# Kernel optimization log

Hardware: AMD Instinct MI355X
Metric: run time of the kernel (lower is better)

The kernel has to match this reference:

```python
import jax, jax.numpy as jnp
import numpy as np

N = 100_000   # nodes
E = 1_600_000 # edges
V = 100_000   # vocab
G = 256       # graphs in batch
D = 64        # emb/hidden dim


def setup_inputs() -> dict:
    key = jax.random.key(0)
    ks = jax.random.split(key, 12)
    x_tokens = jax.random.randint(ks[0], (N, 1), 0, V)
    edge_index = jax.random.randint(ks[1], (2, E), 0, N)
    batch = jnp.sort(jax.random.randint(ks[2], (N,), 0, G))
    s = 0.02
    return {
        "x_tokens": x_tokens,
        "edge_index": edge_index,
        "batch": batch,
        "emb_table": jax.random.normal(ks[3], (V, D), jnp.float32) * s,
        "W0": jax.random.normal(ks[4], (D, D), jnp.float32) * s,
        "b0": jnp.zeros((D,), jnp.float32),
        "W1": jax.random.normal(ks[5], (D, D), jnp.float32) * s,
        "b1": jnp.zeros((D,), jnp.float32),
        "W2": jax.random.normal(ks[6], (D, D), jnp.float32) * s,
        "b2": jnp.zeros((D,), jnp.float32),
        "Wc1": jax.random.normal(ks[7], (2 * D, D), jnp.float32) * s,
        "bc1": jnp.zeros((D,), jnp.float32),
        "Wc2": jax.random.normal(ks[8], (D, 2), jnp.float32) * s,
        "bc2": jnp.zeros((2,), jnp.float32),
    }


def _gcn_norm(edge_index, n_nodes):
    # add self loops, compute symmetric normalization coefficients
    loop = jnp.arange(n_nodes, dtype=edge_index.dtype)
    src = jnp.concatenate([edge_index[0], loop])
    dst = jnp.concatenate([edge_index[1], loop])
    deg = jax.ops.segment_sum(jnp.ones_like(dst, jnp.float32), dst, num_segments=n_nodes)
    dinv = jnp.where(deg > 0, deg ** -0.5, 0.0)
    norm = dinv[src] * dinv[dst]  # [E+N]
    return src, dst, norm


def _gcn_conv(x, W, b, src, dst, norm, n_nodes):
    x = x @ W                                   # [N, D]
    msg = x[src] * norm[:, None]                # gather + scale, [E+N, D]
    out = jax.ops.segment_sum(msg, dst, num_segments=n_nodes)
    return out + b


def reference(x_tokens, edge_index, batch, emb_table, W0, b0, W1, b1, W2, b2, Wc1, bc1, Wc2, bc2):
    n = x_tokens.shape[0]
    src, dst, norm = _gcn_norm(edge_index, n)
    x = emb_table[x_tokens[:, 0]]               # [N, D]
    for W, b in ((W0, b0), (W1, b1), (W2, b2)):
        x = jax.nn.relu(_gcn_conv(x, W, b, src, dst, norm, n))
    # dual pooling over graph ids
    cnt = jax.ops.segment_sum(jnp.ones((n,), x.dtype), batch, num_segments=G)
    h_sum = jax.ops.segment_sum(x, batch, num_segments=G)
    h_mean = h_sum / jnp.maximum(cnt, 1.0)[:, None]
    h_max = jax.ops.segment_max(x, batch, num_segments=G)
    h_max = jnp.where(jnp.isfinite(h_max), h_max, 0.0)
    h = jnp.concatenate([h_mean, h_max], axis=-1)   # [G, 2D]
    logits = jax.nn.relu(h @ Wc1 + bc1) @ Wc2 + bc2  # [G, 2]
    return logits
```

## Files before the change

kernel.cpp:

```cpp
#include <hip/hip_runtime.h>
#include <hip/hip_fp16.h>
#include <math.h>


#define BKT_LOG 9
#define BKT (1 << BKT_LOG)
#define CHUNK 4096

typedef _Float16 h2 __attribute__((ext_vector_type(2)));
typedef _Float16 f16x4 __attribute__((ext_vector_type(4)));
typedef _Float16 f16x8 __attribute__((ext_vector_type(8)));
typedef float f32x2 __attribute__((ext_vector_type(2)));
typedef float f32x4 __attribute__((ext_vector_type(4)));

union HU { unsigned u; h2 h; };
__device__ inline h2 h2bits(unsigned u) { HU x; x.u = u; return x.h; }

#if __has_builtin(__builtin_amdgcn_fdot2)
#define FDOT2(a, b, c) __builtin_amdgcn_fdot2((a), (b), (c), false)
#else
__device__ inline float FDOT2(h2 a, h2 b, float c) {
  return (float)a.x * (float)b.x + (float)a.y * (float)b.y + c;
}
#endif

#define MASK_X 0x00003C00u
#define MASK_Y 0x3C000000u

__device__ inline void acc4c(uint2 v, float& a0, float& a1, float& a2, float& a3) {
  h2 lo = h2bits(v.x), hi = h2bits(v.y);
  a0 = FDOT2(lo, h2bits(MASK_X), a0);
  a1 = FDOT2(lo, h2bits(MASK_Y), a1);
  a2 = FDOT2(hi, h2bits(MASK_X), a2);
  a3 = FDOT2(hi, h2bits(MASK_Y), a3);
}

#if __has_builtin(__builtin_amdgcn_cvt_pk_f32_fp8) && __has_builtin(__builtin_amdgcn_cvt_pk_fp8_f32)
#define HW_FP8 1
#else
#define HW_FP8 0
#endif

__device__ inline float fp8dec_sw(unsigned b) {
  unsigned s = (b >> 7) & 1, e = (b >> 3) & 15, m = b & 7;
  float v;
  if (e == 0) v = (float)m * 0.001953125f;
  else v = __uint_as_float(((e + 120u) << 23) | (m << 20));
  return s ? -v : v;
}
__device__ inline unsigned fp8enc_sw(float f) {
  unsigned s = (__float_as_uint(f) >> 31) << 7;
  float a = fabsf(f);
  if (!(a < 448.f)) return s | 0x7E;
  if (a < 0.0009765625f) return s;
  int e; float m = frexpf(a, &e);
  int E = e + 6;
  unsigned q;
  if (E <= 0) {
    q = (unsigned)lrintf(a * 512.f);
    if (q >= 8) return s | 0x08;
    return s | q;
  }
  q = (unsigned)lrintf((m * 2.f - 1.f) * 8.f);
  if (q == 8) { q = 0; E++; if (E > 15) return s | 0x7E; }
  return s | ((unsigned)E << 3) | q;
}

__device__ inline void acc4fp8(unsigned v, float& a0, float& a1, float& a2, float& a3) {
#if HW_FP8
  f32x2 lo = __builtin_amdgcn_cvt_pk_f32_fp8((int)v, false);
  f32x2 hi = __builtin_amdgcn_cvt_pk_f32_fp8((int)v, true);
  a0 += lo[0]; a1 += lo[1]; a2 += hi[0]; a3 += hi[1];
#else
  a0 += fp8dec_sw(v & 255u);
  a1 += fp8dec_sw((v >> 8) & 255u);
  a2 += fp8dec_sw((v >> 16) & 255u);
  a3 += fp8dec_sw((v >> 24) & 255u);
#endif
}

__device__ inline unsigned pk4fp8(float f0, float f1, float f2, float f3) {
#if HW_FP8
  int t = __builtin_amdgcn_cvt_pk_fp8_f32(f0, f1, 0, false);
  return (unsigned)__builtin_amdgcn_cvt_pk_fp8_f32(f2, f3, t, true);
#else
  return fp8enc_sw(f0) | (fp8enc_sw(f1) << 8) | (fp8enc_sw(f2) << 16) | (fp8enc_sw(f3) << 24);
#endif
}

template <bool F8>
__device__ inline void rows8(const unsigned char* __restrict__ xh, int my,
                             int e0, int e1, int f, int4 iA, int4 iB,
                             float& a0, float& a1, float& a2, float& a3) {
  if (F8) {
    unsigned v0 = 0, v1 = 0, v2 = 0, v3 = 0, v4 = 0, v5 = 0, v6 = 0, v7 = 0;
    if (my + 0 >= e0 && my + 0 < e1) v0 = *(const unsigned*)(xh + ((size_t)(unsigned)iA.x << 6) + f * 4);
    if (my + 1 >= e0 && my + 1 < e1) v1 = *(const unsigned*)(xh + ((size_t)(unsigned)iA.y << 6) + f * 4);
    if (my + 2 >= e0 && my + 2 < e1) v2 = *(const unsigned*)(xh + ((size_t)(unsigned)iA.z << 6) + f * 4);
    if (my + 3 >= e0 && my + 3 < e1) v3 = *(const unsigned*)(xh + ((size_t)(unsigned)iA.w << 6) + f * 4);
    if (my + 4 >= e0 && my + 4 < e1) v4 = *(const unsigned*)(xh + ((size_t)(unsigned)iB.x << 6) + f * 4);
    if (my + 5 >= e0 && my + 5 < e1) v5 = *(const unsigned*)(xh + ((size_t)(unsigned)iB.y << 6) + f * 4);
    if (my + 6 >= e0 && my + 6 < e1) v6 = *(const unsigned*)(xh + ((size_t)(unsigned)iB.z << 6) + f * 4);
    if (my + 7 >= e0 && my + 7 < e1) v7 = *(const unsigned*)(xh + ((size_t)(unsigned)iB.w << 6) + f * 4);
    acc4fp8(v0, a0, a1, a2, a3);
    acc4fp8(v1, a0, a1, a2, a3);
    acc4fp8(v2, a0, a1, a2, a3);
    acc4fp8(v3, a0, a1, a2, a3);
    acc4fp8(v4, a0, a1, a2, a3);
    acc4fp8(v5, a0, a1, a2, a3);
    acc4fp8(v6, a0, a1, a2, a3);
    acc4fp8(v7, a0, a1, a2, a3);
  } else {
    uint2 v0 = {0,0}, v1 = {0,0}, v2 = {0,0}, v3 = {0,0};
    uint2 v4 = {0,0}, v5 = {0,0}, v6 = {0,0}, v7 = {0,0};
    if (my + 0 >= e0 && my + 0 < e1) v0 = *(const uint2*)(xh + ((size_t)(unsigned)iA.x << 7) + f * 8);
    if (my + 1 >= e0 && my + 1 < e1) v1 = *(const uint2*)(xh + ((size_t)(unsigned)iA.y << 7) + f * 8);
    if (my + 2 >= e0 && my + 2 < e1) v2 = *(const uint2*)(xh + ((size_t)(unsigned)iA.z << 7) + f * 8);
    if (my + 3 >= e0 && my + 3 < e1) v3 = *(const uint2*)(xh + ((size_t)(unsigned)iA.w << 7) + f * 8);
    if (my + 4 >= e0 && my + 4 < e1) v4 = *(const uint2*)(xh + ((size_t)(unsigned)iB.x << 7) + f * 8);
    if (my + 5 >= e0 && my + 5 < e1) v5 = *(const uint2*)(xh + ((size_t)(unsigned)iB.y << 7) + f * 8);
    if (my + 6 >= e0 && my + 6 < e1) v6 = *(const uint2*)(xh + ((size_t)(unsigned)iB.z << 7) + f * 8);
    if (my + 7 >= e0 && my + 7 < e1) v7 = *(const uint2*)(xh + ((size_t)(unsigned)iB.w << 7) + f * 8);
    acc4c(v0, a0, a1, a2, a3);
    acc4c(v1, a0, a1, a2, a3);
    acc4c(v2, a0, a1, a2, a3);
    acc4c(v3, a0, a1, a2, a3);
    acc4c(v4, a0, a1, a2, a3);
    acc4c(v5, a0, a1, a2, a3);
    acc4c(v6, a0, a1, a2, a3);
    acc4c(v7, a0, a1, a2, a3);
  }
}

__global__ __launch_bounds__(256) void k_wcvt(const float* __restrict__ W0,
                                              const float* __restrict__ W1,
                                              const float* __restrict__ W2,
                                              _Float16* __restrict__ Wf,
                                              int* __restrict__ gcur,
                                              float* __restrict__ hz, int hzn) {
  if (blockIdx.x < 3) {
    const float* W = (blockIdx.x == 0) ? W0 : (blockIdx.x == 1) ? W1 : W2;
    _Float16* out = Wf + blockIdx.x * 4096;
    for (int i = threadIdx.x; i < 4096; i += 256) {
      int c = i >> 10, s = (i >> 9) & 1, l = (i >> 3) & 63, j = i & 7;
      int k = 32 * s + 8 * (l >> 4) + j;
      int ncol = 16 * c + (l & 15);
      out[i] = (_Float16)W[k * 64 + ncol];
    }
  } else if (blockIdx.x == 3) {
    gcur[threadIdx.x] = 0;
  } else {
    for (int i = threadIdx.x; i < hzn; i += 256) hz[i] = 0.f;
  }
}

__global__ __launch_bounds__(256) void k_part(const int* __restrict__ src,
                                              const int* __restrict__ dst,
                                              int* __restrict__ gcur,
                                              int* __restrict__ ebuf,
                                              int E, int S) {
  __shared__ int pk[CHUNK];
  __shared__ unsigned short bk[CHUNK];
  __shared__ unsigned short sp[CHUNK];
  __shared__ int h[256], sc[256], base[256], cur[256];
  int tid = threadIdx.x;
  long c0 = (long)blockIdx.x * CHUNK;
  int m = (int)min((long)CHUNK, (long)E - c0);
  h[tid] = 0;
  __syncthreads();
  for (int i = tid; i < m; i += 256) {
    int s = src[c0 + i];
    int d = dst[c0 + i];
    int b = d >> BKT_LOG;
    pk[i] = ((d & (BKT - 1)) << 17) | s;
    bk[i] = (unsigned short)b;
    atomicAdd(&h[b], 1);
  }
  __syncthreads();
  int hv = h[tid];
  if (hv) base[tid] = atomicAdd(&gcur[tid], hv);
  sc[tid] = hv;
  __syncthreads();
  for (int d = 1; d < 256; d <<= 1) {
    int t = (tid >= d) ? sc[tid - d] : 0;
    __syncthreads();
    sc[tid] += t;
    __syncthreads();
  }
  cur[tid] = sc[tid] - hv;
  __syncthreads();
  for (int i = tid; i < m; i += 256) {
    int p = atomicAdd(&cur[bk[i]], 1);
    sp[p] = (unsigned short)i;
  }
  __syncthreads();
  for (int j = tid; j < m; j += 256) {
    int lo = 0, hi = 255;
    while (lo < hi) { int mid = (lo + hi) >> 1; if (sc[mid] > j) hi = mid; else lo = mid + 1; }
    int b = lo;
    int rel = j - (sc[b] - h[b]);
    int gpos = base[b] + rel;
    if (gpos < S)
      ebuf[(size_t)b * S + gpos] = pk[sp[j]];
  }
}

__global__ __launch_bounds__(512) void k_bplace(const int* __restrict__ ebuf,
                                                const int* __restrict__ gcur,
                                                int* __restrict__ off,
                                                int* __restrict__ eend,
                                                int* __restrict__ csrc,
                                                float* __restrict__ dinv,
                                                int N, int S) {
  __shared__ int s[512];
  __shared__ int cur[512];
  int b = blockIdx.x, tid = threadIdx.x;
  int n0 = b << BKT_LOG;
  int nn = min(BKT, N - n0);
  int e0 = b * S;
  int cnt = min(gcur[b], S - nn);
  s[tid] = (tid < nn) ? 1 : 0;
  __syncthreads();
  for (int e = tid; e < cnt; e += 512) atomicAdd(&s[ebuf[e0 + e] >> 17], 1);
  __syncthreads();
  int degws = s[tid];
  for (int d = 1; d < 512; d <<= 1) {
    int t = (tid >= d) ? s[tid - d] : 0;
    __syncthreads();
    s[tid] += t;
    __syncthreads();
  }
  int excl = s[tid] - degws;
  if (tid < nn) {
    off[n0 + tid] = e0 + excl;
    eend[n0 + tid] = e0 + excl + degws;
    dinv[n0 + tid] = 1.0f / sqrtf((float)degws);
    csrc[e0 + excl] = n0 + tid;
  }
  cur[tid] = excl + ((tid < nn) ? 1 : 0);
  __syncthreads();
  for (int e = tid; e < cnt; e += 512) {
    int p = ebuf[e0 + e];
    int pos = e0 + atomicAdd(&cur[p >> 17], 1);
    csrc[pos] = p & 0x1FFFF;
  }
}

template <bool EMB, bool F8>
__global__ __launch_bounds__(256) void k_mfmamm(const _Float16* __restrict__ y,
                                                const int* __restrict__ tok,
                                                const float* __restrict__ emb,
                                                const _Float16* __restrict__ Wf,
                                                const float* __restrict__ dinv,
                                                float scale,
                                                unsigned char* __restrict__ xh,
                                                int n) {
  __shared__ _Float16 lds[4 * 16 * 72];
  int w = threadIdx.x >> 6, l = threadIdx.x & 63;
  int m = l & 15, q = l >> 4;
  int rbase = blockIdx.x * 64 + w * 16;

  f16x8 a0, a1;
  if (EMB) {
    int node = min(rbase + m, n - 1);
    const float* er = emb + (size_t)tok[node] * 64;
    float4 v0 = *(const float4*)(er + q * 8);
    float4 v1 = *(const float4*)(er + q * 8 + 4);
    float4 v2 = *(const float4*)(er + 32 + q * 8);
    float4 v3 = *(const float4*)(er + 32 + q * 8 + 4);
    a0[0] = (_Float16)v0.x; a0[1] = (_Float16)v0.y; a0[2] = (_Float16)v0.z; a0[3] = (_Float16)v0.w;
    a0[4] = (_Float16)v1.x; a0[5] = (_Float16)v1.y; a0[6] = (_Float16)v1.z; a0[7] = (_Float16)v1.w;
    a1[0] = (_Float16)v2.x; a1[1] = (_Float16)v2.y; a1[2] = (_Float16)v2.z; a1[3] = (_Float16)v2.w;
    a1[4] = (_Float16)v3.x; a1[5] = (_Float16)v3.y; a1[6] = (_Float16)v3.z; a1[7] = (_Float16)v3.w;
  } else {
    int node = rbase + m;
    const _Float16* yr = y + ((size_t)(unsigned)node << 6);
    a0 = *(const f16x8*)(yr + q * 8);
    a1 = *(const f16x8*)(yr + 32 + q * 8);
  }
  float4 d4 = *(const float4*)(dinv + rbase + q * 4);

  const f16x8* wf = (const f16x8*)Wf + l;
  f32x4 acc[4];
#pragma unroll
  for (int c = 0; c < 4; c++) {
    f32x4 z = {0.f, 0.f, 0.f, 0.f};
    z = __builtin_amdgcn_mfma_f32_16x16x32_f16(a0, wf[(c * 2 + 0) * 64], z, 0, 0, 0);
    z = __builtin_amdgcn_mfma_f32_16x16x32_f16(a1, wf[(c * 2 + 1) * 64], z, 0, 0, 0);
    acc[c] = z;
  }

  const float ds[4] = {d4.x * scale, d4.y * scale, d4.z * scale, d4.w * scale};
  _Float16* ldw = lds + w * 16 * 72;
#pragma unroll
  for (int c = 0; c < 4; c++)
#pragma unroll
    for (int r = 0; r < 4; r++)
      ldw[(q * 4 + r) * 72 + c * 16 + m] = (_Float16)(acc[c][r] * ds[r]);
  __syncthreads();

  int row2 = l & 15, c2 = l >> 4;
  int node = rbase + row2;
  if (node < n) {
    if (F8) {
      const _Float16* sp16 = ldw + row2 * 72 + c2 * 16;
      unsigned wds[4];
#pragma unroll
      for (int k = 0; k < 4; k++)
        wds[k] = pk4fp8((float)sp16[4 * k + 0], (float)sp16[4 * k + 1],
                        (float)sp16[4 * k + 2], (float)sp16[4 * k + 3]);
      uint4 ov; ov.x = wds[0]; ov.y = wds[1]; ov.z = wds[2]; ov.w = wds[3];
      *(uint4*)(xh + ((size_t)(unsigned)node << 6) + c2 * 16) = ov;
    } else {
      const uint4* s4 = (const uint4*)(ldw + row2 * 72 + c2 * 16);
      uint4 v0 = s4[0], v1 = s4[1];
      uint4* dst = (uint4*)(xh + ((size_t)(unsigned)node << 7) + c2 * 32);
      dst[0] = v0;
      dst[1] = v1;
    }
  }
}

template <bool F8>
__global__ __launch_bounds__(256) void k_aggregate(const int* __restrict__ off,
                                                   const int* __restrict__ eend,
                                                   const int* __restrict__ csrc,
                                                   const float* __restrict__ dinv,
                                                   const unsigned char* __restrict__ xh,
                                                   const float* __restrict__ bias,
                                                   float invs,
                                                   _Float16* __restrict__ outp,
                                                   int n, int stride) {
  int lane = threadIdx.x & 63;
  int p = lane >> 4;
  int f = lane & 15;
  int t = __builtin_amdgcn_readfirstlane(blockIdx.x * 4 + (threadIdx.x >> 6));
  if (t >= n) return;

  int e0 = off[t], e1 = eend[t];
  int4 iA = {0, 0, 0, 0}, iB = {0, 0, 0, 0};
  {
    int my = (e0 & ~7) + p * 8;
    if (my < e1) iA = *(const int4*)(csrc + my);
    if (my + 4 < e1) iB = *(const int4*)(csrc + my + 4);
  }
  int tn = t + stride;
  int e0n = 0, e1n = 0;
  if (tn < n) { e0n = off[tn]; e1n = eend[tn]; }

  while (true) {
    int4 iAn = {0, 0, 0, 0}, iBn = {0, 0, 0, 0};
    if (tn < n) {
      int myn = (e0n & ~7) + p * 8;
      if (myn < e1n) iAn = *(const int4*)(csrc + myn);
      if (myn + 4 < e1n) iBn = *(const int4*)(csrc + myn + 4);
    }
    int tnn = tn + stride;
    int e0nn = 0, e1nn = 0;
    if (tnn < n) { e0nn = off[tnn]; e1nn = eend[tnn]; }

    float a0 = 0.f, a1 = 0.f, a2 = 0.f, a3 = 0.f;
    int base0 = e0 & ~7;
    rows8<F8>(xh, base0 + p * 8, e0, e1, f, iA, iB, a0, a1, a2, a3);
    for (int base = base0 + 32; base < e1; base += 32) {
      int my = base + p * 8;
      int4 jA = {0, 0, 0, 0}, jB = {0, 0, 0, 0};
      if (my < e1) jA = *(const int4*)(csrc + my);
      if (my + 4 < e1) jB = *(const int4*)(csrc + my + 4);
      rows8<F8>(xh, my, e0, e1, f, jA, jB, a0, a1, a2, a3);
    }

    a0 += __shfl_xor(a0, 16); a0 += __shfl_xor(a0, 32);
    a1 += __shfl_xor(a1, 16); a1 += __shfl_xor(a1, 32);
    a2 += __shfl_xor(a2, 16); a2 += __shfl_xor(a2, 32);
    a3 += __shfl_xor(a3, 16); a3 += __shfl_xor(a3, 32);
    if (p == 0) {
      float sc = dinv[t] * invs;
      float4 bb = *(const float4*)(bias + f * 4);
      f16x4 hv;
      hv[0] = (_Float16)(fmaxf(a0 * sc + bb.x, 0.f) * 4096.f);
      hv[1] = (_Float16)(fmaxf(a1 * sc + bb.y, 0.f) * 4096.f);
      hv[2] = (_Float16)(fmaxf(a2 * sc + bb.z, 0.f) * 4096.f);
      hv[3] = (_Float16)(fmaxf(a3 * sc + bb.w, 0.f) * 4096.f);
      *(f16x4*)((char*)outp + ((size_t)(unsigned)t << 7) + f * 8) = hv;
    }

    if (tn >= n) break;
    t = tn; e0 = e0n; e1 = e1n; iA = iAn; iB = iBn;
    tn = tnn; e0n = e0nn; e1n = e1nn;
  }
}

__global__ __launch_bounds__(256) void k_pool(const _Float16* __restrict__ x,
                                              const int* __restrict__ batch,
                                              float* __restrict__ hsum,
                                              float* __restrict__ hmax,
                                              int* __restrict__ cntg,
                                              int n) {
  int wid = (blockIdx.x * blockDim.x + threadIdx.x) >> 6;
  int lane = threadIdx.x & 63;
  int i0 = wid * 64;
  if (i0 >= n) return;
  int i1 = min(i0 + 64, n);
  int batch_l = (i0 + lane < n) ? batch[i0 + lane] : 0;
  float gsum = 0.f, gmax = 0.f;
  int cur = __shfl(batch_l, 0);
  int c = 0;
  for (int i = i0; i < i1; i++) {
    int g = __shfl(batch_l, i - i0);
    if (g != cur) {
      atomicAdd(&hsum[cur * 64 + lane], gsum);
      atomicMax((int*)&hmax[cur * 64 + lane], __float_as_int(gmax));
      if (lane == 0) atomicAdd(&cntg[cur], c);
      gsum = 0.f; gmax = 0.f; c = 0; cur = g;
    }
    float v = (float)x[((size_t)(unsigned)i << 6) + lane];
    gsum += v;
    gmax = fmaxf(gmax, v);
    c++;
  }
  atomicAdd(&hsum[cur * 64 + lane], gsum);
  atomicMax((int*)&hmax[cur * 64 + lane], __float_as_int(gmax));
  if (lane == 0) atomicAdd(&cntg[cur], c);
}

__global__ __launch_bounds__(64) void k_cls(const float* __restrict__ hsum,
                                            const float* __restrict__ hmax,
                                            const int* __restrict__ cnt,
                                            const float* __restrict__ Wc1,
                                            const float* __restrict__ bc1,
                                            const float* __restrict__ Wc2,
                                            const float* __restrict__ bc2,
                                            float* __restrict__ out) {
  __shared__ float h[128];
  __shared__ float hid[64];
  int g = blockIdx.x, j = threadIdx.x;
  int c = cnt[g];
  float cf = (float)(c > 0 ? c : 1);
  h[j] = hsum[g * 64 + j] / cf * (1.0f / 4096.0f);
  h[64 + j] = hmax[g * 64 + j] * (1.0f / 4096.0f);
  __syncthreads();
  float acc = bc1[j];
  for (int k = 0; k < 128; k++) acc += h[k] * Wc1[k * 64 + j];
  hid[j] = fmaxf(acc, 0.f);
  __syncthreads();
  if (j < 2) {
    float a = bc2[j];
    for (int k = 0; k < 64; k++) a += hid[k] * Wc2[k * 2 + j];
    out[g * 2 + j] = a;
  }
}

extern "C" void kernel_launch(void* const* d_in, const int* in_sizes, int n_in,
                              void* d_out, int out_size, void* d_ws, size_t ws_size,
                              hipStream_t stream) {
  const int N = in_sizes[0];
  const int E = in_sizes[1] / 2;
  const int G = out_size / 2;
  const int B = (N + BKT - 1) >> BKT_LOG;
  const int Npad = (N + 63) & ~63;
  const int S = ((((E + B - 1) / B) * 3 / 2 + 256) + 7) & ~7;

  const int* tok   = (const int*)d_in[0];
  const int* ei    = (const int*)d_in[1];
  const int* batch = (const int*)d_in[2];
  const float* emb = (const float*)d_in[3];
  const float* W0 = (const float*)d_in[4];  const float* b0 = (const float*)d_in[5];
  const float* W1 = (const float*)d_in[6];  const float* b1 = (const float*)d_in[7];
  const float* W2 = (const float*)d_in[8];  const float* b2 = (const float*)d_in[9];
  const float* Wc1 = (const float*)d_in[10]; const float* bc1 = (const float*)d_in[11];
  const float* Wc2 = (const float*)d_in[12]; const float* bc2 = (const float*)d_in[13];
  const int* srcp = ei;
  const int* dstp = ei + E;

  int* off    = (int*)d_ws;
  int* eend   = off + N;
  float* dinv = (float*)(eend + N);
  int* gcur   = (int*)(dinv + Npad);
  _Float16* Wf = (_Float16*)(gcur + 256);
  int* csrc   = (int*)(Wf + 3 * 4096);
  unsigned char* xh = (unsigned char*)(csrc + (size_t)B * S);
  _Float16* y  = (_Float16*)(xh + (size_t)Npad * 128);
  int* ebuf   = (int*)y;
  float* hsum = (float*)(y + (size_t)Npad * 64);
  float* hmax = hsum + (size_t)G * 64;
  int*   cntg = (int*)(hmax + (size_t)G * 64);

  auto cdiv = [](long a, long b) { return (int)((a + b - 1) / b); };
  const int aggBlocks = 2048;
  const int aggStride = aggBlocks * 4;

  k_wcvt<<<5, 256, 0, stream>>>(W0, W1, W2, Wf, gcur, hsum, G * 129);

  k_part<<<cdiv(E, CHUNK), 256, 0, stream>>>(srcp, dstp, gcur, ebuf, E, S);
  k_bplace<<<B, 512, 0, stream>>>(ebuf, gcur, off, eend, csrc, dinv, N, S);

  k_mfmamm<true, true><<<cdiv(N, 64), 256, 0, stream>>>(nullptr, tok, emb, Wf, dinv, 256.f, xh, N);
  k_aggregate<true><<<aggBlocks, 256, 0, stream>>>(off, eend, csrc, dinv, xh, b0, 1.f / 256.f, y, N, aggStride);

  k_mfmamm<false, true><<<cdiv(N, 64), 256, 0, stream>>>(y, nullptr, nullptr, Wf + 4096, dinv, 1.0f, xh, N);
  k_aggregate<true><<<aggBlocks, 256, 0, stream>>>(off, eend, csrc, dinv, xh, b1, 1.f / 4096.f, y, N, aggStride);

  k_mfmamm<false, false><<<cdiv(N, 64), 256, 0, stream>>>(y, nullptr, nullptr, Wf + 8192, dinv, 1.f / 16.f, xh, N);
  k_aggregate<false><<<aggBlocks, 256, 0, stream>>>(off, eend, csrc, dinv, xh, b2, 1.f / 256.f, y, N, aggStride);

  k_pool<<<cdiv(N, 256), 256, 0, stream>>>(y, batch, hsum, hmax, cntg, N);

  k_cls<<<G, 64, 0, stream>>>(hsum, hmax, cntg, Wc1, bc1, Wc2, bc2, (float*)d_out);
}
```

Before: 304.6 us.

## Fuse graph pooling into final aggregate via atomics and count nodes in bplace

Removes the separate pooling kernel by having the last aggregation layer atomically accumulate per-graph sum and max directly from each node's activations, skipping the fp16 write and reread of the final node features. Node counts per graph are computed with atomics in the CSR placement kernel instead. This trades a launch and a pass over node features for many contended per-node global atomics on a small set of graph addresses, since sorted batch ids make neighboring nodes target the same locations.

```diff
diff --git a/kernel.cpp b/kernel.cpp
--- a/kernel.cpp
+++ b/kernel.cpp
@@ -207,10 +207,12 @@
 
 __global__ __launch_bounds__(512) void k_bplace(const int* __restrict__ ebuf,
                                                 const int* __restrict__ gcur,
+                                                const int* __restrict__ batch,
                                                 int* __restrict__ off,
                                                 int* __restrict__ eend,
                                                 int* __restrict__ csrc,
                                                 float* __restrict__ dinv,
+                                                int* __restrict__ cntg,
                                                 int N, int S) {
   __shared__ int s[512];
   __shared__ int cur[512];
@@ -236,6 +238,7 @@
     eend[n0 + tid] = e0 + excl + degws;
     dinv[n0 + tid] = 1.0f / sqrtf((float)degws);
     csrc[e0 + excl] = n0 + tid;
+    atomicAdd(&cntg[batch[n0 + tid]], 1);
   }
   cur[tid] = excl + ((tid < nn) ? 1 : 0);
   __syncthreads();
@@ -321,7 +324,7 @@
   }
 }
 
-template <bool F8>
+template <bool F8, bool POOL>
 __global__ __launch_bounds__(256) void k_aggregate(const int* __restrict__ off,
                                                    const int* __restrict__ eend,
                                                    const int* __restrict__ csrc,
@@ -330,6 +333,9 @@
                                                    const float* __restrict__ bias,
                                                    float invs,
                                                    _Float16* __restrict__ outp,
+                                                   const int* __restrict__ batch,
+                                                   float* __restrict__ hsum,
+                                                   float* __restrict__ hmax,
                                                    int n, int stride) {
   int lane = threadIdx.x & 63;
   int p = lane >> 4;
@@ -377,51 +383,36 @@
     if (p == 0) {
       float sc = dinv[t] * invs;
       float4 bb = *(const float4*)(bias + f * 4);
-      f16x4 hv;
-      hv[0] = (_Float16)(fmaxf(a0 * sc + bb.x, 0.f) * 4096.f);
-      hv[1] = (_Float16)(fmaxf(a1 * sc + bb.y, 0.f) * 4096.f);
-      hv[2] = (_Float16)(fmaxf(a2 * sc + bb.z, 0.f) * 4096.f);
-      hv[3] = (_Float16)(fmaxf(a3 * sc + bb.w, 0.f) * 4096.f);
-      *(f16x4*)((char*)outp + ((size_t)(unsigned)t << 7) + f * 8) = hv;
+      float v0 = fmaxf(a0 * sc + bb.x, 0.f) * 4096.f;
+      float v1 = fmaxf(a1 * sc + bb.y, 0.f) * 4096.f;
+      float v2 = fmaxf(a2 * sc + bb.z, 0.f) * 4096.f;
+      float v3 = fmaxf(a3 * sc + bb.w, 0.f) * 4096.f;
+      if (POOL) {
+        int g = batch[t];
+        float* hs = hsum + g * 64 + f * 4;
+        int* hm = (int*)(hmax + g * 64 + f * 4);
+        atomicAdd(hs + 0, v0);
+        atomicAdd(hs + 1, v1);
+        atomicAdd(hs + 2, v2);
+        atomicAdd(hs + 3, v3);
+        atomicMax(hm + 0, __float_as_int(v0));
+        atomicMax(hm + 1, __float_as_int(v1));
+        atomicMax(hm + 2, __float_as_int(v2));
+        atomicMax(hm + 3, __float_as_int(v3));
+      } else {
+        f16x4 hv;
+        hv[0] = (_Float16)v0;
+        hv[1] = (_Float16)v1;
+        hv[2] = (_Float16)v2;
+        hv[3] = (_Float16)v3;
+        *(f16x4*)((char*)outp + ((size_t)(unsigned)t << 7) + f * 8) = hv;
+      }
     }
 
     if (tn >= n) break;
     t = tn; e0 = e0n; e1 = e1n; iA = iAn; iB = iBn;
     tn = tnn; e0n = e0nn; e1n = e1nn;
   }
-}
-
-__global__ __launch_bounds__(256) void k_pool(const _Float16* __restrict__ x,
-                                              const int* __restrict__ batch,
-                                              float* __restrict__ hsum,
-                                              float* __restrict__ hmax,
-                                              int* __restrict__ cntg,
-                                              int n) {
-  int wid = (blockIdx.x * blockDim.x + threadIdx.x) >> 6;
-  int lane = threadIdx.x & 63;
-  int i0 = wid * 64;
-  if (i0 >= n) return;
-  int i1 = min(i0 + 64, n);
-  int batch_l = (i0 + lane < n) ? batch[i0 + lane] : 0;
-  float gsum = 0.f, gmax = 0.f;
-  int cur = __shfl(batch_l, 0);
-  int c = 0;
-  for (int i = i0; i < i1; i++) {
-    int g = __shfl(batch_l, i - i0);
-    if (g != cur) {
-      atomicAdd(&hsum[cur * 64 + lane], gsum);
-      atomicMax((int*)&hmax[cur * 64 + lane], __float_as_int(gmax));
-      if (lane == 0) atomicAdd(&cntg[cur], c);
-      gsum = 0.f; gmax = 0.f; c = 0; cur = g;
-    }
-    float v = (float)x[((size_t)(unsigned)i << 6) + lane];
-    gsum += v;
-    gmax = fmaxf(gmax, v);
-    c++;
-  }
-  atomicAdd(&hsum[cur * 64 + lane], gsum);
-  atomicMax((int*)&hmax[cur * 64 + lane], __float_as_int(gmax));
-  if (lane == 0) atomicAdd(&cntg[cur], c);
 }
 
 __global__ __launch_bounds__(64) void k_cls(const float* __restrict__ hsum,
@@ -493,18 +484,16 @@
   k_wcvt<<<5, 256, 0, stream>>>(W0, W1, W2, Wf, gcur, hsum, G * 129);
 
   k_part<<<cdiv(E, CHUNK), 256, 0, stream>>>(srcp, dstp, gcur, ebuf, E, S);
-  k_bplace<<<B, 512, 0, stream>>>(ebuf, gcur, off, eend, csrc, dinv, N, S);
+  k_bplace<<<B, 512, 0, stream>>>(ebuf, gcur, batch, off, eend, csrc, dinv, cntg, N, S);
 
   k_mfmamm<true, true><<<cdiv(N, 64), 256, 0, stream>>>(nullptr, tok, emb, Wf, dinv, 256.f, xh, N);
-  k_aggregate<true><<<aggBlocks, 256, 0, stream>>>(off, eend, csrc, dinv, xh, b0, 1.f / 256.f, y, N, aggStride);
+  k_aggregate<true, false><<<aggBlocks, 256, 0, stream>>>(off, eend, csrc, dinv, xh, b0, 1.f / 256.f, y, nullptr, nullptr, nullptr, N, aggStride);
 
   k_mfmamm<false, true><<<cdiv(N, 64), 256, 0, stream>>>(y, nullptr, nullptr, Wf + 4096, dinv, 1.0f, xh, N);
-  k_aggregate<true><<<aggBlocks, 256, 0, stream>>>(off, eend, csrc, dinv, xh, b1, 1.f / 4096.f, y, N, aggStride);
+  k_aggregate<true, false><<<aggBlocks, 256, 0, stream>>>(off, eend, csrc, dinv, xh, b1, 1.f / 4096.f, y, nullptr, nullptr, nullptr, N, aggStride);
 
   k_mfmamm<false, false><<<cdiv(N, 64), 256, 0, stream>>>(y, nullptr, nullptr, Wf + 8192, dinv, 1.f / 16.f, xh, N);
-  k_aggregate<false><<<aggBlocks, 256, 0, stream>>>(off, eend, csrc, dinv, xh, b2, 1.f / 256.f, y, N, aggStride);
-
-  k_pool<<<cdiv(N, 256), 256, 0, stream>>>(y, batch, hsum, hmax, cntg, N);
+  k_aggregate<false, true><<<aggBlocks, 256, 0, stream>>>(off, eend, csrc, dinv, xh, b2, 1.f / 256.f, nullptr, batch, hsum, hmax, N, aggStride);
 
   k_cls<<<G, 64, 0, stream>>>(hsum, hmax, cntg, Wc1, bc1, Wc2, bc2, (float*)d_out);
 }
```

New measurement: 726.4 us. +138.4%, slower.

## Fuse aggregation with next layer's MFMA matmul into one kernel

Applied to the files above, without the earlier changes.

Adds a k_aggmm kernel. Each wave aggregates neighbour features for 16 nodes, writes the ReLU'd fp16 results into LDS, and then runs the next layer's 64x64 weight multiply with MFMA directly from that tile. This removes the round trip of the intermediate y tensor through global memory and two kernel launches. Buffers are reorganised so the layer outputs ping-pong between separate regions. The trade-offs are lower parallelism: one tile per block, a serial loop over 16 nodes per wave, and extra __syncthreads calls.

```diff
diff --git a/kernel.cpp b/kernel.cpp
--- a/kernel.cpp
+++ b/kernel.cpp
@@ -321,6 +321,126 @@
   }
 }
 
+template <bool F8IN, bool F8OUT>
+__global__ __launch_bounds__(256) void k_aggmm(const int* __restrict__ off,
+                                               const int* __restrict__ eend,
+                                               const int* __restrict__ csrc,
+                                               const float* __restrict__ dinv,
+                                               const unsigned char* __restrict__ xin,
+                                               const float* __restrict__ bias,
+                                               float invs,
+                                               const _Float16* __restrict__ Wf,
+                                               float scale,
+                                               unsigned char* __restrict__ xout,
+                                               int n, int ntiles) {
+  __shared__ _Float16 lds[4 * 2 * 16 * 72];
+  int w = threadIdx.x >> 6, lane = threadIdx.x & 63;
+  int p = lane >> 4, f = lane & 15;
+  _Float16* ytile = lds + w * (2 * 16 * 72);
+  _Float16* ldw   = ytile + 16 * 72;
+  const f16x8* wf = (const f16x8*)Wf + lane;
+
+  for (int tile = blockIdx.x; tile < ntiles; tile += gridDim.x) {
+    int base = tile * 64 + w * 16;
+    int nd = base + f;
+    int e0v = 0, e1v = 0;
+    if (nd < n) { e0v = off[nd]; e1v = eend[nd]; }
+
+    int e0 = __shfl(e0v, 0), e1 = __shfl(e1v, 0);
+    int4 iA = {0, 0, 0, 0}, iB = {0, 0, 0, 0};
+    {
+      int my = (e0 & ~7) + p * 8;
+      if (my < e1) iA = *(const int4*)(csrc + my);
+      if (my + 4 < e1) iB = *(const int4*)(csrc + my + 4);
+    }
+#pragma unroll 1
+    for (int i = 0; i < 16; ++i) {
+      int e0n = 0, e1n = 0;
+      int4 iAn = {0, 0, 0, 0}, iBn = {0, 0, 0, 0};
+      if (i < 15) {
+        e0n = __shfl(e0v, i + 1);
+        e1n = __shfl(e1v, i + 1);
+        int myn = (e0n & ~7) + p * 8;
+        if (myn < e1n) iAn = *(const int4*)(csrc + myn);
+        if (myn + 4 < e1n) iBn = *(const int4*)(csrc + myn + 4);
+      }
+      float a0 = 0.f, a1 = 0.f, a2 = 0.f, a3 = 0.f;
+      int base0 = e0 & ~7;
+      rows8<F8IN>(xin, base0 + p * 8, e0, e1, f, iA, iB, a0, a1, a2, a3);
+      for (int bs = base0 + 32; bs < e1; bs += 32) {
+        int my = bs + p * 8;
+        int4 jA = {0, 0, 0, 0}, jB = {0, 0, 0, 0};
+        if (my < e1) jA = *(const int4*)(csrc + my);
+        if (my + 4 < e1) jB = *(const int4*)(csrc + my + 4);
+        rows8<F8IN>(xin, my, e0, e1, f, jA, jB, a0, a1, a2, a3);
+      }
+      a0 += __shfl_xor(a0, 16); a0 += __shfl_xor(a0, 32);
+      a1 += __shfl_xor(a1, 16); a1 += __shfl_xor(a1, 32);
+      a2 += __shfl_xor(a2, 16); a2 += __shfl_xor(a2, 32);
+      a3 += __shfl_xor(a3, 16); a3 += __shfl_xor(a3, 32);
+      if (p == 0) {
+        int t = __builtin_amdgcn_readfirstlane(base + i);
+        float sc = (t < n ? dinv[t] : 0.f) * invs;
+        float4 bb = *(const float4*)(bias + f * 4);
+        f16x4 hv;
+        hv[0] = (_Float16)(fmaxf(a0 * sc + bb.x, 0.f) * 4096.f);
+        hv[1] = (_Float16)(fmaxf(a1 * sc + bb.y, 0.f) * 4096.f);
+        hv[2] = (_Float16)(fmaxf(a2 * sc + bb.z, 0.f) * 4096.f);
+        hv[3] = (_Float16)(fmaxf(a3 * sc + bb.w, 0.f) * 4096.f);
+        *(f16x4*)(ytile + i * 72 + f * 4) = hv;
+      }
+      e0 = e0n; e1 = e1n; iA = iAn; iB = iBn;
+    }
+    __syncthreads();
+
+    int m = f, q = p;
+    f16x8 A0 = *(const f16x8*)(ytile + m * 72 + q * 8);
+    f16x8 A1 = *(const f16x8*)(ytile + m * 72 + 32 + q * 8);
+    float4 d4;
+    d4.x = (base + q * 4 + 0 < n) ? dinv[base + q * 4 + 0] : 0.f;
+    d4.y = (base + q * 4 + 1 < n) ? dinv[base + q * 4 + 1] : 0.f;
+    d4.z = (base + q * 4 + 2 < n) ? dinv[base + q * 4 + 2] : 0.f;
+    d4.w = (base + q * 4 + 3 < n) ? dinv[base + q * 4 + 3] : 0.f;
+
+    f32x4 acc[4];
+#pragma unroll
+    for (int c = 0; c < 4; c++) {
+      f32x4 z = {0.f, 0.f, 0.f, 0.f};
+      z = __builtin_amdgcn_mfma_f32_16x16x32_f16(A0, wf[(c * 2 + 0) * 64], z, 0, 0, 0);
+      z = __builtin_amdgcn_mfma_f32_16x16x32_f16(A1, wf[(c * 2 + 1) * 64], z, 0, 0, 0);
+      acc[c] = z;
+    }
+    const float ds[4] = {d4.x * scale, d4.y * scale, d4.z * scale, d4.w * scale};
+#pragma unroll
+    for (int c = 0; c < 4; c++)
+#pragma unroll
+      for (int r = 0; r < 4; r++)
+        ldw[(q * 4 + r) * 72 + c * 16 + m] = (_Float16)(acc[c][r] * ds[r]);
+    __syncthreads();
+
+    int row2 = lane & 15, c2 = lane >> 4;
+    int node = base + row2;
+    if (node < n) {
+      if (F8OUT) {
+        const _Float16* sp16 = ldw + row2 * 72 + c2 * 16;
+        unsigned wds[4];
+#pragma unroll
+        for (int k = 0; k < 4; k++)
+          wds[k] = pk4fp8((float)sp16[4 * k + 0], (float)sp16[4 * k + 1],
+                          (float)sp16[4 * k + 2], (float)sp16[4 * k + 3]);
+        uint4 ov; ov.x = wds[0]; ov.y = wds[1]; ov.z = wds[2]; ov.w = wds[3];
+        *(uint4*)(xout + ((size_t)(unsigned)node << 6) + c2 * 16) = ov;
+      } else {
+        const uint4* s4 = (const uint4*)(ldw + row2 * 72 + c2 * 16);
+        uint4 v0 = s4[0], v1 = s4[1];
+        uint4* dst = (uint4*)(xout + ((size_t)(unsigned)node << 7) + c2 * 32);
+        dst[0] = v0;
+        dst[1] = v1;
+      }
+    }
+  }
+}
+
 template <bool F8>
 __global__ __launch_bounds__(256) void k_aggregate(const int* __restrict__ off,
                                                    const int* __restrict__ eend,
@@ -479,14 +599,18 @@
   int* gcur   = (int*)(dinv + Npad);
   _Float16* Wf = (_Float16*)(gcur + 256);
   int* csrc   = (int*)(Wf + 3 * 4096);
-  unsigned char* xh = (unsigned char*)(csrc + (size_t)B * S);
-  _Float16* y  = (_Float16*)(xh + (size_t)Npad * 128);
-  int* ebuf   = (int*)y;
-  float* hsum = (float*)(y + (size_t)Npad * 64);
+  unsigned char* X = (unsigned char*)(csrc + (size_t)B * S);
+  unsigned char* xh_a = X;
+  unsigned char* xh_b = X + (size_t)Npad * 64;
+  unsigned char* yreg = X + (size_t)Npad * 128;
+  unsigned char* xh_c = yreg;
+  int* ebuf   = (int*)yreg;
+  float* hsum = (float*)(yreg + (size_t)Npad * 128);
   float* hmax = hsum + (size_t)G * 64;
   int*   cntg = (int*)(hmax + (size_t)G * 64);
 
   auto cdiv = [](long a, long b) { return (int)((a + b - 1) / b); };
+  const int ntiles = cdiv(N, 64);
   const int aggBlocks = 2048;
   const int aggStride = aggBlocks * 4;
 
@@ -495,16 +619,18 @@
   k_part<<<cdiv(E, CHUNK), 256, 0, stream>>>(srcp, dstp, gcur, ebuf, E, S);
   k_bplace<<<B, 512, 0, stream>>>(ebuf, gcur, off, eend, csrc, dinv, N, S);
 
-  k_mfmamm<true, true><<<cdiv(N, 64), 256, 0, stream>>>(nullptr, tok, emb, Wf, dinv, 256.f, xh, N);
-  k_aggregate<true><<<aggBlocks, 256, 0, stream>>>(off, eend, csrc, dinv, xh, b0, 1.f / 256.f, y, N, aggStride);
-
-  k_mfmamm<false, true><<<cdiv(N, 64), 256, 0, stream>>>(y, nullptr, nullptr, Wf + 4096, dinv, 1.0f, xh, N);
-  k_aggregate<true><<<aggBlocks, 256, 0, stream>>>(off, eend, csrc, dinv, xh, b1, 1.f / 4096.f, y, N, aggStride);
-
-  k_mfmamm<false, false><<<cdiv(N, 64), 256, 0, stream>>>(y, nullptr, nullptr, Wf + 8192, dinv, 1.f / 16.f, xh, N);
-  k_aggregate<false><<<aggBlocks, 256, 0, stream>>>(off, eend, csrc, dinv, xh, b2, 1.f / 256.f, y, N, aggStride);
-
-  k_pool<<<cdiv(N, 256), 256, 0, stream>>>(y, batch, hsum, hmax, cntg, N);
+  k_mfmamm<true, true><<<ntiles, 256, 0, stream>>>(nullptr, tok, emb, Wf, dinv, 256.f, xh_a, N);
+
+  k_aggmm<true, true><<<ntiles, 256, 0, stream>>>(off, eend, csrc, dinv, xh_a, b0, 1.f / 256.f,
+                                                  Wf + 4096, 1.0f, xh_b, N, ntiles);
+
+  k_aggmm<true, false><<<ntiles, 256, 0, stream>>>(off, eend, csrc, dinv, xh_b, b1, 1.f / 4096.f,
+                                                   Wf + 8192, 1.f / 16.f, xh_c, N, ntiles);
+
+  k_aggregate<false><<<aggBlocks, 256, 0, stream>>>(off, eend, csrc, dinv, xh_c, b2, 1.f / 256.f,
+                                                    (_Float16*)X, N, aggStride);
+
+  k_pool<<<cdiv(N, 256), 256, 0, stream>>>((const _Float16*)X, batch, hsum, hmax, cntg, N);
 
   k_cls<<<G, 64, 0, stream>>>(hsum, hmax, cntg, Wc1, bc1, Wc2, bc2, (float*)d_out);
 }
```

Result: slower. 323.8 us (+6.3%).
